# Kernel optimization log

Measured on AMD Instinct MI355X. Metric: run time of the kernel, lower is better.

The kernel has to match this reference:

```python
import jax, jax.numpy as jnp
import numpy as np

W_RNN = 768
DEC_H = 256
TAGS = 2
TAG_EM = 32


def setup_inputs() -> dict:
    key = jax.random.key(0)
    ks = jax.random.split(key, 8)
    B, T = 64, 512
    in_size = W_RNN + TAG_EM  # 800
    aff_in = W_RNN + DEC_H    # 1024
    sents_vec = jax.random.normal(ks[0], (B, T, W_RNN), dtype=jnp.float32)
    mask_cls = jnp.ones((B, T), dtype=jnp.float32)
    # xavier-uniform-ish init for weights, zeros for biases (matches param_init)
    def xavier(k, shape):
        fan_in, fan_out = shape[1], shape[0]
        lim = float(np.sqrt(6.0 / (fan_in + fan_out)))
        return jax.random.uniform(k, shape, jnp.float32, -lim, lim)
    Wih = xavier(ks[1], (4 * DEC_H, in_size))
    Whh = xavier(ks[2], (4 * DEC_H, DEC_H))
    bih = jnp.zeros((4 * DEC_H,), jnp.float32)
    bhh = jnp.zeros((4 * DEC_H,), jnp.float32)
    Waff = xavier(ks[3], (TAGS, aff_in))
    baff = jnp.zeros((TAGS,), jnp.float32)
    tag_em = xavier(ks[4], (TAGS, TAG_EM))
    return {"sents_vec": sents_vec, "mask_cls": mask_cls, "Wih": Wih,
            "Whh": Whh, "bih": bih, "bhh": bhh, "Waff": Waff,
            "baff": baff, "tag_em": tag_em}


def reference(sents_vec, mask_cls, Wih, Whh, bih, bhh, Waff, baff, tag_em):
    # Dropout is treated in eval mode (identity), as is standard for a
    # deterministic correctness baseline.
    B, T, D = sents_vec.shape
    H = DEC_H
    h0 = jnp.zeros((B, H), sents_vec.dtype)
    go = jnp.zeros((B, TAG_EM), sents_vec.dtype)

    Hs = jnp.swapaxes(sents_vec, 0, 1)        # [T, B, D]
    Ms = jnp.swapaxes(mask_cls, 0, 1)[..., None]  # [T, B, 1]

    def step(carry, xs):
        h, c, yem = carry
        Hi, mi = xs
        x = jnp.concatenate([yem, Hi], axis=1)            # [B, 800]
        gates = x @ Wih.T + h @ Whh.T + (bih + bhh)       # [B, 4H]
        i_g, f_g, g_g, o_g = jnp.split(gates, 4, axis=1)  # torch LSTMCell order
        c_new = jax.nn.sigmoid(f_g) * c + jax.nn.sigmoid(i_g) * jnp.tanh(g_g)
        h_new = jax.nn.sigmoid(o_g) * jnp.tanh(c_new)
        score = jnp.concatenate([h_new, Hi], axis=1) @ Waff.T + baff  # [B, TAGS]
        pred = jnp.argmax(score, axis=-1)                 # [B]
        yem_new = tag_em[pred]                            # [B, TAG_EM]
        h_out = h_new * mi + h * (1.0 - mi)
        c_out = c_new * mi + c * (1.0 - mi)
        return (h_out, c_out, yem_new), score

    _, scores = jax.lax.scan(step, (h0, h0, go), (Hs, Ms))  # [T, B, TAGS]
    scores = jnp.swapaxes(scores, 0, 1)                      # [B, T, TAGS]
    return jax.nn.log_softmax(scores, axis=2)
```

## Files before the change

kernel.cpp:

```cpp
#include <hip/hip_runtime.h>
#include <cstdint>
#include <cstddef>

#define TT 512
#define BB 64
#define HH 256
#define NG 1024
#define DI 768
#define KY 32

#define LDP 56

typedef __attribute__((ext_vector_type(8))) short bfrag_t;
typedef __attribute__((ext_vector_type(4))) float f4_t;

__device__ __forceinline__ float sigf(float x) {
    return __fdividef(1.f, 1.f + __expf(-x));
}
__device__ __forceinline__ float tanhfast(float x) {
    return fmaf(2.f, sigf(2.f * x), -1.f);
}
__device__ __forceinline__ unsigned short bf_hi(float x) {
    return (unsigned short)(__float_as_uint(x) >> 16);
}
__device__ __forceinline__ float bf_hi_f(float x) {
    return __uint_as_float(__float_as_uint(x) & 0xffff0000u);
}

__global__ __launch_bounds__(256) void kgemm2(
    const float* __restrict__ sents, const float* __restrict__ Wih,
    const float* __restrict__ bih, const float* __restrict__ bhh,
    float* __restrict__ gpre, int t0)
{
    __shared__ unsigned short Ah[128 * LDP], Al[128 * LDP];
    __shared__ unsigned short Bh[128 * LDP], Bl[128 * LDP];

    const int tid = threadIdx.x;
    const int nb = blockIdx.x;
    const int mb = blockIdx.y;
    const int wv = tid >> 6, lane = tid & 63;
    const int wm = (wv >> 1) * 64, wn = (wv & 1) * 64;
    const int fl = lane & 15, quad = lane >> 4;

    f4_t acc[4][4];
#pragma unroll
    for (int mi = 0; mi < 4; ++mi)
#pragma unroll
        for (int ni = 0; ni < 4; ++ni) acc[mi][ni] = (f4_t)0.f;

    const int sr = tid >> 1, sk = (tid & 1) * 16;
    const int gr = mb * 128 + sr;
    const float* aptr = sents + ((size_t)(gr & 63) * TT + t0 + (gr >> 6)) * DI + sk;
    const float* bptr = Wih + (size_t)(nb * 128 + sr) * 800 + KY + sk;

    for (int k0 = 0; k0 < DI; k0 += 32) {
        float4 av[4], bv[4];
#pragma unroll
        for (int i = 0; i < 4; ++i) {
            av[i] = *(const float4*)(aptr + k0 + i * 4);
            bv[i] = *(const float4*)(bptr + k0 + i * 4);
        }
        __syncthreads();
#pragma unroll
        for (int i = 0; i < 4; ++i) {
            ushort4 h4, l4;
            h4.x = bf_hi(av[i].x); l4.x = bf_hi(av[i].x - bf_hi_f(av[i].x));
            h4.y = bf_hi(av[i].y); l4.y = bf_hi(av[i].y - bf_hi_f(av[i].y));
            h4.z = bf_hi(av[i].z); l4.z = bf_hi(av[i].z - bf_hi_f(av[i].z));
            h4.w = bf_hi(av[i].w); l4.w = bf_hi(av[i].w - bf_hi_f(av[i].w));
            *(ushort4*)&Ah[sr * LDP + sk + i * 4] = h4;
            *(ushort4*)&Al[sr * LDP + sk + i * 4] = l4;
            h4.x = bf_hi(bv[i].x); l4.x = bf_hi(bv[i].x - bf_hi_f(bv[i].x));
            h4.y = bf_hi(bv[i].y); l4.y = bf_hi(bv[i].y - bf_hi_f(bv[i].y));
            h4.z = bf_hi(bv[i].z); l4.z = bf_hi(bv[i].z - bf_hi_f(bv[i].z));
            h4.w = bf_hi(bv[i].w); l4.w = bf_hi(bv[i].w - bf_hi_f(bv[i].w));
            *(ushort4*)&Bh[sr * LDP + sk + i * 4] = h4;
            *(ushort4*)&Bl[sr * LDP + sk + i * 4] = l4;
        }
        __syncthreads();

        bfrag_t ah[4], al2[4], bh[4], bl2[4];
#pragma unroll
        for (int mi = 0; mi < 4; ++mi) {
            int row = wm + mi * 16 + fl;
            ah[mi]  = *(const bfrag_t*)&Ah[row * LDP + quad * 8];
            al2[mi] = *(const bfrag_t*)&Al[row * LDP + quad * 8];
        }
#pragma unroll
        for (int ni = 0; ni < 4; ++ni) {
            int col = wn + ni * 16 + fl;
            bh[ni]  = *(const bfrag_t*)&Bh[col * LDP + quad * 8];
            bl2[ni] = *(const bfrag_t*)&Bl[col * LDP + quad * 8];
        }
#pragma unroll
        for (int mi = 0; mi < 4; ++mi)
#pragma unroll
            for (int ni = 0; ni < 4; ++ni) {
                acc[mi][ni] = __builtin_amdgcn_mfma_f32_16x16x32_bf16(
                    ah[mi], bh[ni], acc[mi][ni], 0, 0, 0);
                acc[mi][ni] = __builtin_amdgcn_mfma_f32_16x16x32_bf16(
                    ah[mi], bl2[ni], acc[mi][ni], 0, 0, 0);
                acc[mi][ni] = __builtin_amdgcn_mfma_f32_16x16x32_bf16(
                    al2[mi], bh[ni], acc[mi][ni], 0, 0, 0);
            }
    }

#pragma unroll
    for (int ni = 0; ni < 4; ++ni) {
        int gcol = nb * 128 + wn + ni * 16 + fl;
        float bias = bih[gcol] + bhh[gcol];
#pragma unroll
        for (int mi = 0; mi < 4; ++mi) {
            int grow = mb * 128 + wm + mi * 16 + quad * 4;
#pragma unroll
            for (int r = 0; r < 4; ++r)
                gpre[(size_t)(grow + r) * NG + gcol] = acc[mi][ni][r] + bias;
        }
    }
}

__global__ __launch_bounds__(256) void kshi(
    const float* __restrict__ sents, const float* __restrict__ Waff,
    const float* __restrict__ baff, float* __restrict__ shi, int t0)
{
    const int tid = threadIdx.x;
    const int lane = tid & 63;
    const int r = blockIdx.x * 4 + (tid >> 6);
    const int b = r & 63, tl = r >> 6;
    const float* hi = sents + ((size_t)b * TT + t0 + tl) * DI;
    float p0 = 0.f, p1 = 0.f;
#pragma unroll
    for (int kk = 0; kk < 12; ++kk) {
        int k = kk * 64 + lane;
        float x = hi[k];
        p0 = fmaf(x, Waff[HH + k], p0);
        p1 = fmaf(x, Waff[NG + HH + k], p1);
    }
#pragma unroll
    for (int off = 32; off >= 1; off >>= 1) {
        p0 += __shfl_xor(p0, off, 64);
        p1 += __shfl_xor(p1, off, 64);
    }
    if (lane == 0) {
        shi[(size_t)r * 2 + 0] = p0 + baff[0];
        shi[(size_t)r * 2 + 1] = p1 + baff[1];
    }
}

__global__ void kinit(unsigned long long* __restrict__ hbox) {
    hbox[(size_t)blockIdx.x * 512 + threadIdx.x] = 0ull;
}

__global__ __launch_bounds__(512, 1) void krec3(
    const float* __restrict__ gpre,
    const float* __restrict__ shi,
    const float* __restrict__ Whh,
    const float* __restrict__ mask,
    float* __restrict__ out,
    float* __restrict__ sh, float* __restrict__ sc, int* __restrict__ sp,
    unsigned long long* __restrict__ hbox,
    const float* __restrict__ Wih, const float* __restrict__ tag,
    const float* __restrict__ Waff,
    int t0, int Tc, int first)
{
    const int blk = blockIdx.x;
    const int g = blk >> 6, b = blk & 63;
    const int tid = threadIdx.x;
    const int w = tid >> 6, lane = tid & 63;
    const int jl = lane & 7, kq = lane >> 3;
    const int jh = w * 8 + jl;
    const int jglob = g * 64 + jh;

    __shared__ float hk[8 * 36];
    __shared__ float hnS[HH];
    __shared__ float P[2][4][64];
    __shared__ float tg[2][KY];
    __shared__ float red[8][2];

    float4 wreg[4][8];
#pragma unroll
    for (int gt = 0; gt < 4; ++gt) {
        const float4* src = (const float4*)(Whh + (size_t)(gt * HH + jglob) * HH + kq * 32);
#pragma unroll
        for (int kk = 0; kk < 8; ++kk) wreg[gt][kk] = src[kk];
    }

    const int sdim = w * 32 + (lane & 31);
    const int stag = lane >> 5;
    const float waffR = Waff[(size_t)stag * NG + sdim];

    if (tid < 2 * KY) tg[tid >> 5][tid & 31] = tag[tid];
    __syncthreads();
    {
        int r = tid >> 8, rem = tid & 255, gt = rem >> 6, j2 = rem & 63;
        int row = gt * HH + g * 64 + j2;
        const float4* wr = (const float4*)(Wih + (size_t)row * 800);
        float s = 0.f;
#pragma unroll
        for (int kk = 0; kk < 8; ++kk) {
            float4 v = wr[kk];
            s = fmaf(v.x, tg[r][kk * 4 + 0], s);
            s = fmaf(v.y, tg[r][kk * 4 + 1], s);
            s = fmaf(v.z, tg[r][kk * 4 + 2], s);
            s = fmaf(v.w, tg[r][kk * 4 + 3], s);
        }
        P[r][gt][j2] = s;
    }

    float creg; int pred;
    if (first) {
        creg = 0.f; pred = -1;
        if (tid < 72) ((float4*)hk)[tid] = make_float4(0.f, 0.f, 0.f, 0.f);
    } else {
        creg = sc[(size_t)b * HH + jglob];
        pred = sp[b];
        if (tid < HH) hk[(tid >> 5) * 36 + (tid & 31)] = sh[(size_t)b * HH + tid];
    }
    __syncthreads();

    float cgp0, cgp1, cgp2, cgp3, cmi, cs0, cs1;
    {
        const float* gp = gpre + ((size_t)0 * BB + b) * NG;
        cgp0 = gp[0 * HH + jglob]; cgp1 = gp[1 * HH + jglob];
        cgp2 = gp[2 * HH + jglob]; cgp3 = gp[3 * HH + jglob];
        cmi = mask[(size_t)b * TT + t0];
        const float* s2 = shi + ((size_t)0 * BB + b) * 2;
        cs0 = s2[0]; cs1 = s2[1];
    }

    for (int tl = 0; tl < Tc; ++tl) {
        const int t = t0 + tl;
        const int p = t & 1;

        float pv0 = 0.f, pv1 = 0.f, pv2 = 0.f, pv3 = 0.f;
        if (pred >= 0) {
            pv0 = P[pred][0][jh]; pv1 = P[pred][1][jh];
            pv2 = P[pred][2][jh]; pv3 = P[pred][3][jh];
        }

        float a0 = 0.f, a1 = 0.f, a2 = 0.f, a3 = 0.f;
        const float4* h4 = (const float4*)(hk + kq * 36);
#pragma unroll
        for (int kk = 0; kk < 8; ++kk) {
            float4 hv = h4[kk];
            a0 = fmaf(wreg[0][kk].x, hv.x, a0); a0 = fmaf(wreg[0][kk].y, hv.y, a0);
            a0 = fmaf(wreg[0][kk].z, hv.z, a0); a0 = fmaf(wreg[0][kk].w, hv.w, a0);
            a1 = fmaf(wreg[1][kk].x, hv.x, a1); a1 = fmaf(wreg[1][kk].y, hv.y, a1);
            a1 = fmaf(wreg[1][kk].z, hv.z, a1); a1 = fmaf(wreg[1][kk].w, hv.w, a1);
            a2 = fmaf(wreg[2][kk].x, hv.x, a2); a2 = fmaf(wreg[2][kk].y, hv.y, a2);
            a2 = fmaf(wreg[2][kk].z, hv.z, a2); a2 = fmaf(wreg[2][kk].w, hv.w, a2);
            a3 = fmaf(wreg[3][kk].x, hv.x, a3); a3 = fmaf(wreg[3][kk].y, hv.y, a3);
            a3 = fmaf(wreg[3][kk].z, hv.z, a3); a3 = fmaf(wreg[3][kk].w, hv.w, a3);
        }
        a0 += __shfl_xor(a0, 8, 64); a0 += __shfl_xor(a0, 16, 64); a0 += __shfl_xor(a0, 32, 64);
        a1 += __shfl_xor(a1, 8, 64); a1 += __shfl_xor(a1, 16, 64); a1 += __shfl_xor(a1, 32, 64);
        a2 += __shfl_xor(a2, 8, 64); a2 += __shfl_xor(a2, 16, 64); a2 += __shfl_xor(a2, 32, 64);
        a3 += __shfl_xor(a3, 8, 64); a3 += __shfl_xor(a3, 16, 64); a3 += __shfl_xor(a3, 32, 64);

        float gi = a0 + cgp0 + pv0;
        float gf = a1 + cgp1 + pv1;
        float gg = a2 + cgp2 + pv2;
        float go = a3 + cgp3 + pv3;
        float ig = sigf(gi), fg = sigf(gf);
        float g2 = tanhfast(gg), og = sigf(go);
        float cn = fmaf(fg, creg, ig * g2);
        float hn = og * tanhfast(cn);
        float mi = cmi;
        float s2v0 = cs0, s2v1 = cs1;
        creg = cn * mi + creg * (1.f - mi);

        if (kq == 0) {
            unsigned long long wd =
                ((unsigned long long)__float_as_uint(hn) << 32) | (unsigned)(t + 1);
            __hip_atomic_store(&hbox[((size_t)(p * BB + b) * 4 + g) * 64 + jh], wd,
                               __ATOMIC_RELAXED, __HIP_MEMORY_SCOPE_AGENT);
            hnS[jglob] = hn;
        }

        if (tl + 1 < Tc) {
            const float* gp2 = gpre + ((size_t)(tl + 1) * BB + b) * NG;
            cgp0 = gp2[0 * HH + jglob]; cgp1 = gp2[1 * HH + jglob];
            cgp2 = gp2[2 * HH + jglob]; cgp3 = gp2[3 * HH + jglob];
            cmi = mask[(size_t)b * TT + t + 1];
            const float* s2n = shi + ((size_t)(tl + 1) * BB + b) * 2;
            cs0 = s2n[0]; cs1 = s2n[1];
        }

        if (tid < 192) {
            int pg = (g + 1 + (tid >> 6)) & 3, j2 = tid & 63;
            const unsigned long long* wp = &hbox[((size_t)(p * BB + b) * 4 + pg) * 64 + j2];
            unsigned long long wv;
            do {
                wv = __hip_atomic_load(wp, __ATOMIC_RELAXED, __HIP_MEMORY_SCOPE_AGENT);
            } while ((unsigned)wv != (unsigned)(t + 1));
            hnS[pg * 64 + j2] = __uint_as_float((unsigned)(wv >> 32));
        }
        __syncthreads();

        if (tid < HH) {
            int idx = (tid >> 5) * 36 + (tid & 31);
            float hold = hk[idx];
            hk[idx] = hnS[tid] * mi + hold * (1.f - mi);
        }
        float prod = hnS[sdim] * waffR;
        prod += __shfl_xor(prod, 1, 64);
        prod += __shfl_xor(prod, 2, 64);
        prod += __shfl_xor(prod, 4, 64);
        prod += __shfl_xor(prod, 8, 64);
        prod += __shfl_xor(prod, 16, 64);
        if ((lane & 31) == 0) red[w][stag] = prod;
        __syncthreads();

        float s0 = red[0][0];
        s0 += red[1][0]; s0 += red[2][0]; s0 += red[3][0];
        s0 += red[4][0]; s0 += red[5][0]; s0 += red[6][0]; s0 += red[7][0];
        float s1 = red[0][1];
        s1 += red[1][1]; s1 += red[2][1]; s1 += red[3][1];
        s1 += red[4][1]; s1 += red[5][1]; s1 += red[6][1]; s1 += red[7][1];
        float ts0 = s0 + s2v0, ts1 = s1 + s2v1;
        pred = (ts1 > ts0) ? 1 : 0;
        if (g == 0 && tid == 0) {
            float m = fmaxf(ts0, ts1);
            float lse = m + log1pf(expf(-fabsf(ts0 - ts1)));
            float* op = out + ((size_t)b * TT + t) * 2;
            op[0] = ts0 - lse; op[1] = ts1 - lse;
        }
    }

    if (kq == 0) {
        sh[(size_t)b * HH + jglob] = hk[(jglob >> 5) * 36 + (jglob & 31)];
        sc[(size_t)b * HH + jglob] = creg;
    }
    if (g == 0 && tid == 0) sp[b] = pred;
}

extern "C" void kernel_launch(void* const* d_in, const int* in_sizes, int n_in,
                              void* d_out, int out_size, void* d_ws, size_t ws_size,
                              hipStream_t stream) {
    (void)in_sizes; (void)n_in; (void)out_size;
    const float* sents = (const float*)d_in[0];
    const float* mask  = (const float*)d_in[1];
    const float* Wih   = (const float*)d_in[2];
    const float* Whh   = (const float*)d_in[3];
    const float* bih   = (const float*)d_in[4];
    const float* bhh   = (const float*)d_in[5];
    const float* Waff  = (const float*)d_in[6];
    const float* baff  = (const float*)d_in[7];
    const float* tag   = (const float*)d_in[8];
    float* out = (float*)d_out;

    const size_t fixed = (size_t)BB * HH * 4 * 2
                       + BB * 4
                       + (size_t)2 * BB * 4 * 64 * 8
                       + 4096;
    int Tc = 8;
    const int cands[7] = {512, 256, 128, 64, 32, 16, 8};
    for (int i = 0; i < 7; ++i) {
        size_t need = (size_t)cands[i] * BB * NG * 4
                    + (size_t)cands[i] * BB * 2 * 4
                    + fixed;
        if (need <= ws_size) { Tc = cands[i]; break; }
    }

    char* wsp = (char*)d_ws;
    float* gpre = (float*)wsp; wsp += (size_t)Tc * BB * NG * 4;
    float* shiw = (float*)wsp; wsp += (size_t)Tc * BB * 2 * 4;
    float* shst = (float*)wsp; wsp += (size_t)BB * HH * 4;
    float* scst = (float*)wsp; wsp += (size_t)BB * HH * 4;
    int*   spst = (int*)wsp;   wsp += BB * 4;
    unsigned long long* hbox = (unsigned long long*)wsp;

    kinit<<<dim3(64), 512, 0, stream>>>(hbox);

    const int nch = TT / Tc;
    for (int c = 0; c < nch; ++c) {
        const int t0 = c * Tc;
        kgemm2<<<dim3(8, Tc * 64 / 128), 256, 0, stream>>>(sents, Wih, bih, bhh, gpre, t0);
        kshi<<<dim3(Tc * 16), 256, 0, stream>>>(sents, Waff, baff, shiw, t0);
        krec3<<<dim3(256), 512, 0, stream>>>(gpre, shiw, Whh, mask, out,
                                             shst, scst, spst, hbox,
                                             Wih, tag, Waff, t0, Tc, (c == 0) ? 1 : 0);
    }
}
```

Before: 1.289 ms.

## Fuse next-chunk input GEMM and score projection into the recurrence launch

Replaces the per-chunk sequence of three kernels (input-gate GEMM, tag-score projection, recurrence) with one kernel launch per chunk. Blocks 0-255 run the recurrence for the current chunk while the extra blocks compute the GEMM and score projection for the next chunk into double-buffered workspace. The aim is to hide the input-projection work behind the latency-bound serial recurrence. In exchange, chunk size is capped at 32 steps, which means more launches and repeated per-chunk setup (Whh register reload, P table). The merged kernel may also raise register pressure. The cross-block spin-wait relies on the 256 recurrence blocks all being resident at the same time, which depends on them being dispatched first.

```diff
diff --git a/kernel.cpp b/kernel.cpp
--- a/kernel.cpp
+++ b/kernel.cpp
@@ -151,187 +151,303 @@
     hbox[(size_t)blockIdx.x * 512 + threadIdx.x] = 0ull;
 }
 
-__global__ __launch_bounds__(512, 1) void krec3(
-    const float* __restrict__ gpre,
-    const float* __restrict__ shi,
-    const float* __restrict__ Whh,
-    const float* __restrict__ mask,
+__global__ __launch_bounds__(512, 1) void kstep(
+    const float* __restrict__ sents,
+    const float* __restrict__ Wih, const float* __restrict__ bih,
+    const float* __restrict__ bhh, const float* __restrict__ Whh,
+    const float* __restrict__ mask, const float* __restrict__ Waff,
+    const float* __restrict__ baff, const float* __restrict__ tag,
     float* __restrict__ out,
+    const float* __restrict__ gpreR, float* __restrict__ gpreW,
+    const float* __restrict__ shiR, float* __restrict__ shiW,
     float* __restrict__ sh, float* __restrict__ sc, int* __restrict__ sp,
     unsigned long long* __restrict__ hbox,
-    const float* __restrict__ Wih, const float* __restrict__ tag,
-    const float* __restrict__ Waff,
-    int t0, int Tc, int first)
+    int t0, int Tc, int first, int doNext)
 {
-    const int blk = blockIdx.x;
-    const int g = blk >> 6, b = blk & 63;
+    __shared__ union {
+        struct { unsigned short Ah[128 * LDP], Al[128 * LDP],
+                                Bh[128 * LDP], Bl[128 * LDP]; } g;
+        struct { float hk[8 * 36]; float hnS[HH]; float P[2][4][64];
+                 float tg[2][KY]; float red[8][2]; } r;
+    } sm;
+
     const int tid = threadIdx.x;
-    const int w = tid >> 6, lane = tid & 63;
-    const int jl = lane & 7, kq = lane >> 3;
-    const int jh = w * 8 + jl;
-    const int jglob = g * 64 + jh;
-
-    __shared__ float hk[8 * 36];
-    __shared__ float hnS[HH];
-    __shared__ float P[2][4][64];
-    __shared__ float tg[2][KY];
-    __shared__ float red[8][2];
-
-    float4 wreg[4][8];
-#pragma unroll
-    for (int gt = 0; gt < 4; ++gt) {
-        const float4* src = (const float4*)(Whh + (size_t)(gt * HH + jglob) * HH + kq * 32);
-#pragma unroll
-        for (int kk = 0; kk < 8; ++kk) wreg[gt][kk] = src[kk];
-    }
-
-    const int sdim = w * 32 + (lane & 31);
-    const int stag = lane >> 5;
-    const float waffR = Waff[(size_t)stag * NG + sdim];
-
-    if (tid < 2 * KY) tg[tid >> 5][tid & 31] = tag[tid];
-    __syncthreads();
-    {
-        int r = tid >> 8, rem = tid & 255, gt = rem >> 6, j2 = rem & 63;
-        int row = gt * HH + g * 64 + j2;
-        const float4* wr = (const float4*)(Wih + (size_t)row * 800);
-        float s = 0.f;
-#pragma unroll
-        for (int kk = 0; kk < 8; ++kk) {
-            float4 v = wr[kk];
-            s = fmaf(v.x, tg[r][kk * 4 + 0], s);
-            s = fmaf(v.y, tg[r][kk * 4 + 1], s);
-            s = fmaf(v.z, tg[r][kk * 4 + 2], s);
-            s = fmaf(v.w, tg[r][kk * 4 + 3], s);
-        }
-        P[r][gt][j2] = s;
-    }
-
-    float creg; int pred;
-    if (first) {
-        creg = 0.f; pred = -1;
-        if (tid < 72) ((float4*)hk)[tid] = make_float4(0.f, 0.f, 0.f, 0.f);
+    const int gemmBase = 256;
+    const int shiBase  = 256 + Tc * 4;
+
+    if (blockIdx.x < 256) {
+        const int blk = blockIdx.x;
+        const int g = blk >> 6, b = blk & 63;
+        const int w = tid >> 6, lane = tid & 63;
+        const int jl = lane & 7, kq = lane >> 3;
+        const int jh = w * 8 + jl;
+        const int jglob = g * 64 + jh;
+
+        float4 wreg[4][8];
+#pragma unroll
+        for (int gt = 0; gt < 4; ++gt) {
+            const float4* src = (const float4*)(Whh + (size_t)(gt * HH + jglob) * HH + kq * 32);
+#pragma unroll
+            for (int kk = 0; kk < 8; ++kk) wreg[gt][kk] = src[kk];
+        }
+
+        const int sdim = w * 32 + (lane & 31);
+        const int stag = lane >> 5;
+        const float waffR = Waff[(size_t)stag * NG + sdim];
+
+        if (tid < 2 * KY) sm.r.tg[tid >> 5][tid & 31] = tag[tid];
+        __syncthreads();
+        {
+            int r = tid >> 8, rem = tid & 255, gt = rem >> 6, j2 = rem & 63;
+            int row = gt * HH + g * 64 + j2;
+            const float4* wr = (const float4*)(Wih + (size_t)row * 800);
+            float s = 0.f;
+#pragma unroll
+            for (int kk = 0; kk < 8; ++kk) {
+                float4 v = wr[kk];
+                s = fmaf(v.x, sm.r.tg[r][kk * 4 + 0], s);
+                s = fmaf(v.y, sm.r.tg[r][kk * 4 + 1], s);
+                s = fmaf(v.z, sm.r.tg[r][kk * 4 + 2], s);
+                s = fmaf(v.w, sm.r.tg[r][kk * 4 + 3], s);
+            }
+            sm.r.P[r][gt][j2] = s;
+        }
+
+        float creg; int pred;
+        if (first) {
+            creg = 0.f; pred = -1;
+            if (tid < 72) ((float4*)sm.r.hk)[tid] = make_float4(0.f, 0.f, 0.f, 0.f);
+        } else {
+            creg = sc[(size_t)b * HH + jglob];
+            pred = sp[b];
+            if (tid < HH) sm.r.hk[(tid >> 5) * 36 + (tid & 31)] = sh[(size_t)b * HH + tid];
+        }
+        __syncthreads();
+
+        float cgp0, cgp1, cgp2, cgp3, cmi, cs0, cs1;
+        {
+            const float* gp = gpreR + (size_t)b * NG;
+            cgp0 = gp[0 * HH + jglob]; cgp1 = gp[1 * HH + jglob];
+            cgp2 = gp[2 * HH + jglob]; cgp3 = gp[3 * HH + jglob];
+            cmi = mask[(size_t)b * TT + t0];
+            const float* s2 = shiR + (size_t)b * 2;
+            cs0 = s2[0]; cs1 = s2[1];
+        }
+
+        for (int tl = 0; tl < Tc; ++tl) {
+            const int t = t0 + tl;
+            const int p = t & 1;
+
+            float pv0 = 0.f, pv1 = 0.f, pv2 = 0.f, pv3 = 0.f;
+            if (pred >= 0) {
+                pv0 = sm.r.P[pred][0][jh]; pv1 = sm.r.P[pred][1][jh];
+                pv2 = sm.r.P[pred][2][jh]; pv3 = sm.r.P[pred][3][jh];
+            }
+
+            float a0 = 0.f, a1 = 0.f, a2 = 0.f, a3 = 0.f;
+            const float4* h4 = (const float4*)(sm.r.hk + kq * 36);
+#pragma unroll
+            for (int kk = 0; kk < 8; ++kk) {
+                float4 hv = h4[kk];
+                a0 = fmaf(wreg[0][kk].x, hv.x, a0); a0 = fmaf(wreg[0][kk].y, hv.y, a0);
+                a0 = fmaf(wreg[0][kk].z, hv.z, a0); a0 = fmaf(wreg[0][kk].w, hv.w, a0);
+                a1 = fmaf(wreg[1][kk].x, hv.x, a1); a1 = fmaf(wreg[1][kk].y, hv.y, a1);
+                a1 = fmaf(wreg[1][kk].z, hv.z, a1); a1 = fmaf(wreg[1][kk].w, hv.w, a1);
+                a2 = fmaf(wreg[2][kk].x, hv.x, a2); a2 = fmaf(wreg[2][kk].y, hv.y, a2);
+                a2 = fmaf(wreg[2][kk].z, hv.z, a2); a2 = fmaf(wreg[2][kk].w, hv.w, a2);
+                a3 = fmaf(wreg[3][kk].x, hv.x, a3); a3 = fmaf(wreg[3][kk].y, hv.y, a3);
+                a3 = fmaf(wreg[3][kk].z, hv.z, a3); a3 = fmaf(wreg[3][kk].w, hv.w, a3);
+            }
+            a0 += __shfl_xor(a0, 8, 64); a0 += __shfl_xor(a0, 16, 64); a0 += __shfl_xor(a0, 32, 64);
+            a1 += __shfl_xor(a1, 8, 64); a1 += __shfl_xor(a1, 16, 64); a1 += __shfl_xor(a1, 32, 64);
+            a2 += __shfl_xor(a2, 8, 64); a2 += __shfl_xor(a2, 16, 64); a2 += __shfl_xor(a2, 32, 64);
+            a3 += __shfl_xor(a3, 8, 64); a3 += __shfl_xor(a3, 16, 64); a3 += __shfl_xor(a3, 32, 64);
+
+            float gi = a0 + cgp0 + pv0;
+            float gf = a1 + cgp1 + pv1;
+            float gg = a2 + cgp2 + pv2;
+            float go = a3 + cgp3 + pv3;
+            float ig = sigf(gi), fg = sigf(gf);
+            float g2 = tanhfast(gg), og = sigf(go);
+            float cn = fmaf(fg, creg, ig * g2);
+            float hn = og * tanhfast(cn);
+            float mi = cmi;
+            float s2v0 = cs0, s2v1 = cs1;
+            creg = cn * mi + creg * (1.f - mi);
+
+            if (kq == 0) {
+                unsigned long long wd =
+                    ((unsigned long long)__float_as_uint(hn) << 32) | (unsigned)(t + 1);
+                __hip_atomic_store(&hbox[((size_t)(p * BB + b) * 4 + g) * 64 + jh], wd,
+                                   __ATOMIC_RELAXED, __HIP_MEMORY_SCOPE_AGENT);
+                sm.r.hnS[jglob] = hn;
+            }
+
+            if (tl + 1 < Tc) {
+                const float* gp2 = gpreR + ((size_t)(tl + 1) * BB + b) * NG;
+                cgp0 = gp2[0 * HH + jglob]; cgp1 = gp2[1 * HH + jglob];
+                cgp2 = gp2[2 * HH + jglob]; cgp3 = gp2[3 * HH + jglob];
+                cmi = mask[(size_t)b * TT + t + 1];
+                const float* s2n = shiR + ((size_t)(tl + 1) * BB + b) * 2;
+                cs0 = s2n[0]; cs1 = s2n[1];
+            }
+
+            if (tid < 192) {
+                int pg = (g + 1 + (tid >> 6)) & 3, j2 = tid & 63;
+                const unsigned long long* wp = &hbox[((size_t)(p * BB + b) * 4 + pg) * 64 + j2];
+                unsigned long long wv;
+                do {
+                    wv = __hip_atomic_load(wp, __ATOMIC_RELAXED, __HIP_MEMORY_SCOPE_AGENT);
+                } while ((unsigned)wv != (unsigned)(t + 1));
+                sm.r.hnS[pg * 64 + j2] = __uint_as_float((unsigned)(wv >> 32));
+            }
+            __syncthreads();
+
+            if (tid < HH) {
+                int idx = (tid >> 5) * 36 + (tid & 31);
+                float hold = sm.r.hk[idx];
+                sm.r.hk[idx] = sm.r.hnS[tid] * mi + hold * (1.f - mi);
+            }
+            float prod = sm.r.hnS[sdim] * waffR;
+            prod += __shfl_xor(prod, 1, 64);
+            prod += __shfl_xor(prod, 2, 64);
+            prod += __shfl_xor(prod, 4, 64);
+            prod += __shfl_xor(prod, 8, 64);
+            prod += __shfl_xor(prod, 16, 64);
+            if ((lane & 31) == 0) sm.r.red[w][stag] = prod;
+            __syncthreads();
+
+            float s0 = sm.r.red[0][0];
+            s0 += sm.r.red[1][0]; s0 += sm.r.red[2][0]; s0 += sm.r.red[3][0];
+            s0 += sm.r.red[4][0]; s0 += sm.r.red[5][0]; s0 += sm.r.red[6][0]; s0 += sm.r.red[7][0];
+            float s1 = sm.r.red[0][1];
+            s1 += sm.r.red[1][1]; s1 += sm.r.red[2][1]; s1 += sm.r.red[3][1];
+            s1 += sm.r.red[4][1]; s1 += sm.r.red[5][1]; s1 += sm.r.red[6][1]; s1 += sm.r.red[7][1];
+            float ts0 = s0 + s2v0, ts1 = s1 + s2v1;
+            pred = (ts1 > ts0) ? 1 : 0;
+            if (g == 0 && tid == 0) {
+                float m = fmaxf(ts0, ts1);
+                float lse = m + log1pf(expf(-fabsf(ts0 - ts1)));
+                float* op = out + ((size_t)b * TT + t) * 2;
+                op[0] = ts0 - lse; op[1] = ts1 - lse;
+            }
+        }
+
+        if (kq == 0) {
+            sh[(size_t)b * HH + jglob] = sm.r.hk[(jglob >> 5) * 36 + (jglob & 31)];
+            sc[(size_t)b * HH + jglob] = creg;
+        }
+        if (g == 0 && tid == 0) sp[b] = pred;
+
+    } else if (blockIdx.x < shiBase) {
+        if (!doNext) return;
+        const int gb = blockIdx.x - gemmBase;
+        const int nb = gb & 7, mb = gb >> 3;
+        const int t0n = t0 + Tc;
+        const int wv = tid >> 6, lane = tid & 63;
+        const int wm = (wv >> 2) * 64, wn = (wv & 3) * 32;
+        const int fl = lane & 15, quad = lane >> 4;
+
+        f4_t acc[4][2];
+#pragma unroll
+        for (int mi = 0; mi < 4; ++mi)
+#pragma unroll
+            for (int ni = 0; ni < 2; ++ni) acc[mi][ni] = (f4_t)0.f;
+
+        const int sr = tid >> 2, sk = (tid & 3) * 8;
+        const int gr = mb * 128 + sr;
+        const float* aptr = sents + ((size_t)(gr & 63) * TT + t0n + (gr >> 6)) * DI + sk;
+        const float* bptr = Wih + (size_t)(nb * 128 + sr) * 800 + KY + sk;
+
+        for (int k0 = 0; k0 < DI; k0 += 32) {
+            float4 av[2], bv[2];
+            av[0] = *(const float4*)(aptr + k0);
+            av[1] = *(const float4*)(aptr + k0 + 4);
+            bv[0] = *(const float4*)(bptr + k0);
+            bv[1] = *(const float4*)(bptr + k0 + 4);
+            __syncthreads();
+#pragma unroll
+            for (int i = 0; i < 2; ++i) {
+                ushort4 h4, l4;
+                h4.x = bf_hi(av[i].x); l4.x = bf_hi(av[i].x - bf_hi_f(av[i].x));
+                h4.y = bf_hi(av[i].y); l4.y = bf_hi(av[i].y - bf_hi_f(av[i].y));
+                h4.z = bf_hi(av[i].z); l4.z = bf_hi(av[i].z - bf_hi_f(av[i].z));
+                h4.w = bf_hi(av[i].w); l4.w = bf_hi(av[i].w - bf_hi_f(av[i].w));
+                *(ushort4*)&sm.g.Ah[sr * LDP + sk + i * 4] = h4;
+                *(ushort4*)&sm.g.Al[sr * LDP + sk + i * 4] = l4;
+                h4.x = bf_hi(bv[i].x); l4.x = bf_hi(bv[i].x - bf_hi_f(bv[i].x));
+                h4.y = bf_hi(bv[i].y); l4.y = bf_hi(bv[i].y - bf_hi_f(bv[i].y));
+                h4.z = bf_hi(bv[i].z); l4.z = bf_hi(bv[i].z - bf_hi_f(bv[i].z));
+                h4.w = bf_hi(bv[i].w); l4.w = bf_hi(bv[i].w - bf_hi_f(bv[i].w));
+                *(ushort4*)&sm.g.Bh[sr * LDP + sk + i * 4] = h4;
+                *(ushort4*)&sm.g.Bl[sr * LDP + sk + i * 4] = l4;
+            }
+            __syncthreads();
+
+            bfrag_t ah[4], al2[4], bh[2], bl2[2];
+#pragma unroll
+            for (int mi = 0; mi < 4; ++mi) {
+                int row = wm + mi * 16 + fl;
+                ah[mi]  = *(const bfrag_t*)&sm.g.Ah[row * LDP + quad * 8];
+                al2[mi] = *(const bfrag_t*)&sm.g.Al[row * LDP + quad * 8];
+            }
+#pragma unroll
+            for (int ni = 0; ni < 2; ++ni) {
+                int col = wn + ni * 16 + fl;
+                bh[ni]  = *(const bfrag_t*)&sm.g.Bh[col * LDP + quad * 8];
+                bl2[ni] = *(const bfrag_t*)&sm.g.Bl[col * LDP + quad * 8];
+            }
+#pragma unroll
+            for (int mi = 0; mi < 4; ++mi)
+#pragma unroll
+                for (int ni = 0; ni < 2; ++ni) {
+                    acc[mi][ni] = __builtin_amdgcn_mfma_f32_16x16x32_bf16(
+                        ah[mi], bh[ni], acc[mi][ni], 0, 0, 0);
+                    acc[mi][ni] = __builtin_amdgcn_mfma_f32_16x16x32_bf16(
+                        ah[mi], bl2[ni], acc[mi][ni], 0, 0, 0);
+                    acc[mi][ni] = __builtin_amdgcn_mfma_f32_16x16x32_bf16(
+                        al2[mi], bh[ni], acc[mi][ni], 0, 0, 0);
+                }
+        }
+
+#pragma unroll
+        for (int ni = 0; ni < 2; ++ni) {
+            int gcol = nb * 128 + wn + ni * 16 + fl;
+            float bias = bih[gcol] + bhh[gcol];
+#pragma unroll
+            for (int mi = 0; mi < 4; ++mi) {
+                int grow = mb * 128 + wm + mi * 16 + quad * 4;
+#pragma unroll
+                for (int r = 0; r < 4; ++r)
+                    gpreW[(size_t)(grow + r) * NG + gcol] = acc[mi][ni][r] + bias;
+            }
+        }
+
     } else {
-        creg = sc[(size_t)b * HH + jglob];
-        pred = sp[b];
-        if (tid < HH) hk[(tid >> 5) * 36 + (tid & 31)] = sh[(size_t)b * HH + tid];
-    }
-    __syncthreads();
-
-    float cgp0, cgp1, cgp2, cgp3, cmi, cs0, cs1;
-    {
-        const float* gp = gpre + ((size_t)0 * BB + b) * NG;
-        cgp0 = gp[0 * HH + jglob]; cgp1 = gp[1 * HH + jglob];
-        cgp2 = gp[2 * HH + jglob]; cgp3 = gp[3 * HH + jglob];
-        cmi = mask[(size_t)b * TT + t0];
-        const float* s2 = shi + ((size_t)0 * BB + b) * 2;
-        cs0 = s2[0]; cs1 = s2[1];
-    }
-
-    for (int tl = 0; tl < Tc; ++tl) {
-        const int t = t0 + tl;
-        const int p = t & 1;
-
-        float pv0 = 0.f, pv1 = 0.f, pv2 = 0.f, pv3 = 0.f;
-        if (pred >= 0) {
-            pv0 = P[pred][0][jh]; pv1 = P[pred][1][jh];
-            pv2 = P[pred][2][jh]; pv3 = P[pred][3][jh];
-        }
-
-        float a0 = 0.f, a1 = 0.f, a2 = 0.f, a3 = 0.f;
-        const float4* h4 = (const float4*)(hk + kq * 36);
-#pragma unroll
-        for (int kk = 0; kk < 8; ++kk) {
-            float4 hv = h4[kk];
-            a0 = fmaf(wreg[0][kk].x, hv.x, a0); a0 = fmaf(wreg[0][kk].y, hv.y, a0);
-            a0 = fmaf(wreg[0][kk].z, hv.z, a0); a0 = fmaf(wreg[0][kk].w, hv.w, a0);
-            a1 = fmaf(wreg[1][kk].x, hv.x, a1); a1 = fmaf(wreg[1][kk].y, hv.y, a1);
-            a1 = fmaf(wreg[1][kk].z, hv.z, a1); a1 = fmaf(wreg[1][kk].w, hv.w, a1);
-            a2 = fmaf(wreg[2][kk].x, hv.x, a2); a2 = fmaf(wreg[2][kk].y, hv.y, a2);
-            a2 = fmaf(wreg[2][kk].z, hv.z, a2); a2 = fmaf(wreg[2][kk].w, hv.w, a2);
-            a3 = fmaf(wreg[3][kk].x, hv.x, a3); a3 = fmaf(wreg[3][kk].y, hv.y, a3);
-            a3 = fmaf(wreg[3][kk].z, hv.z, a3); a3 = fmaf(wreg[3][kk].w, hv.w, a3);
-        }
-        a0 += __shfl_xor(a0, 8, 64); a0 += __shfl_xor(a0, 16, 64); a0 += __shfl_xor(a0, 32, 64);
-        a1 += __shfl_xor(a1, 8, 64); a1 += __shfl_xor(a1, 16, 64); a1 += __shfl_xor(a1, 32, 64);
-        a2 += __shfl_xor(a2, 8, 64); a2 += __shfl_xor(a2, 16, 64); a2 += __shfl_xor(a2, 32, 64);
-        a3 += __shfl_xor(a3, 8, 64); a3 += __shfl_xor(a3, 16, 64); a3 += __shfl_xor(a3, 32, 64);
-
-        float gi = a0 + cgp0 + pv0;
-        float gf = a1 + cgp1 + pv1;
-        float gg = a2 + cgp2 + pv2;
-        float go = a3 + cgp3 + pv3;
-        float ig = sigf(gi), fg = sigf(gf);
-        float g2 = tanhfast(gg), og = sigf(go);
-        float cn = fmaf(fg, creg, ig * g2);
-        float hn = og * tanhfast(cn);
-        float mi = cmi;
-        float s2v0 = cs0, s2v1 = cs1;
-        creg = cn * mi + creg * (1.f - mi);
-
-        if (kq == 0) {
-            unsigned long long wd =
-                ((unsigned long long)__float_as_uint(hn) << 32) | (unsigned)(t + 1);
-            __hip_atomic_store(&hbox[((size_t)(p * BB + b) * 4 + g) * 64 + jh], wd,
-                               __ATOMIC_RELAXED, __HIP_MEMORY_SCOPE_AGENT);
-            hnS[jglob] = hn;
-        }
-
-        if (tl + 1 < Tc) {
-            const float* gp2 = gpre + ((size_t)(tl + 1) * BB + b) * NG;
-            cgp0 = gp2[0 * HH + jglob]; cgp1 = gp2[1 * HH + jglob];
-            cgp2 = gp2[2 * HH + jglob]; cgp3 = gp2[3 * HH + jglob];
-            cmi = mask[(size_t)b * TT + t + 1];
-            const float* s2n = shi + ((size_t)(tl + 1) * BB + b) * 2;
-            cs0 = s2n[0]; cs1 = s2n[1];
-        }
-
-        if (tid < 192) {
-            int pg = (g + 1 + (tid >> 6)) & 3, j2 = tid & 63;
-            const unsigned long long* wp = &hbox[((size_t)(p * BB + b) * 4 + pg) * 64 + j2];
-            unsigned long long wv;
-            do {
-                wv = __hip_atomic_load(wp, __ATOMIC_RELAXED, __HIP_MEMORY_SCOPE_AGENT);
-            } while ((unsigned)wv != (unsigned)(t + 1));
-            hnS[pg * 64 + j2] = __uint_as_float((unsigned)(wv >> 32));
-        }
-        __syncthreads();
-
-        if (tid < HH) {
-            int idx = (tid >> 5) * 36 + (tid & 31);
-            float hold = hk[idx];
-            hk[idx] = hnS[tid] * mi + hold * (1.f - mi);
-        }
-        float prod = hnS[sdim] * waffR;
-        prod += __shfl_xor(prod, 1, 64);
-        prod += __shfl_xor(prod, 2, 64);
-        prod += __shfl_xor(prod, 4, 64);
-        prod += __shfl_xor(prod, 8, 64);
-        prod += __shfl_xor(prod, 16, 64);
-        if ((lane & 31) == 0) red[w][stag] = prod;
-        __syncthreads();
-
-        float s0 = red[0][0];
-        s0 += red[1][0]; s0 += red[2][0]; s0 += red[3][0];
-        s0 += red[4][0]; s0 += red[5][0]; s0 += red[6][0]; s0 += red[7][0];
-        float s1 = red[0][1];
-        s1 += red[1][1]; s1 += red[2][1]; s1 += red[3][1];
-        s1 += red[4][1]; s1 += red[5][1]; s1 += red[6][1]; s1 += red[7][1];
-        float ts0 = s0 + s2v0, ts1 = s1 + s2v1;
-        pred = (ts1 > ts0) ? 1 : 0;
-        if (g == 0 && tid == 0) {
-            float m = fmaxf(ts0, ts1);
-            float lse = m + log1pf(expf(-fabsf(ts0 - ts1)));
-            float* op = out + ((size_t)b * TT + t) * 2;
-            op[0] = ts0 - lse; op[1] = ts1 - lse;
-        }
-    }
-
-    if (kq == 0) {
-        sh[(size_t)b * HH + jglob] = hk[(jglob >> 5) * 36 + (jglob & 31)];
-        sc[(size_t)b * HH + jglob] = creg;
-    }
-    if (g == 0 && tid == 0) sp[b] = pred;
+        if (!doNext) return;
+        const int wv = tid >> 6, lane = tid & 63;
+        const int r = (blockIdx.x - shiBase) * 8 + wv;
+        const int b = r & 63, tl = r >> 6;
+        const int t0n = t0 + Tc;
+        const float* hi = sents + ((size_t)b * TT + t0n + tl) * DI;
+        float p0 = 0.f, p1 = 0.f;
+#pragma unroll
+        for (int kk = 0; kk < 12; ++kk) {
+            int k = kk * 64 + lane;
+            float x = hi[k];
+            p0 = fmaf(x, Waff[HH + k], p0);
+            p1 = fmaf(x, Waff[NG + HH + k], p1);
+        }
+#pragma unroll
+        for (int off = 32; off >= 1; off >>= 1) {
+            p0 += __shfl_xor(p0, off, 64);
+            p1 += __shfl_xor(p1, off, 64);
+        }
+        if (lane == 0) {
+            shiW[(size_t)r * 2 + 0] = p0 + baff[0];
+            shiW[(size_t)r * 2 + 1] = p1 + baff[1];
+        }
+    }
 }
 
 extern "C" void kernel_launch(void* const* d_in, const int* in_sizes, int n_in,
@@ -354,31 +470,38 @@
                        + (size_t)2 * BB * 4 * 64 * 8
                        + 4096;
     int Tc = 8;
-    const int cands[7] = {512, 256, 128, 64, 32, 16, 8};
-    for (int i = 0; i < 7; ++i) {
-        size_t need = (size_t)cands[i] * BB * NG * 4
-                    + (size_t)cands[i] * BB * 2 * 4
+    const int cands[4] = {32, 16, 8, 4};
+    for (int i = 0; i < 4; ++i) {
+        size_t need = 2 * ((size_t)cands[i] * BB * NG * 4 + (size_t)cands[i] * BB * 2 * 4)
                     + fixed;
         if (need <= ws_size) { Tc = cands[i]; break; }
     }
 
     char* wsp = (char*)d_ws;
-    float* gpre = (float*)wsp; wsp += (size_t)Tc * BB * NG * 4;
-    float* shiw = (float*)wsp; wsp += (size_t)Tc * BB * 2 * 4;
+    float* gpre0 = (float*)wsp; wsp += (size_t)Tc * BB * NG * 4;
+    float* gpre1 = (float*)wsp; wsp += (size_t)Tc * BB * NG * 4;
+    float* shi0 = (float*)wsp; wsp += (size_t)Tc * BB * 2 * 4;
+    float* shi1 = (float*)wsp; wsp += (size_t)Tc * BB * 2 * 4;
     float* shst = (float*)wsp; wsp += (size_t)BB * HH * 4;
     float* scst = (float*)wsp; wsp += (size_t)BB * HH * 4;
     int*   spst = (int*)wsp;   wsp += BB * 4;
     unsigned long long* hbox = (unsigned long long*)wsp;
 
+    float* gbuf[2] = {gpre0, gpre1};
+    float* sbuf[2] = {shi0, shi1};
+
     kinit<<<dim3(64), 512, 0, stream>>>(hbox);
+    kgemm2<<<dim3(8, Tc * 64 / 128), 256, 0, stream>>>(sents, Wih, bih, bhh, gpre0, 0);
+    kshi<<<dim3(Tc * 16), 256, 0, stream>>>(sents, Waff, baff, shi0, 0);
 
     const int nch = TT / Tc;
+    const int grid = 256 + Tc * 4 + Tc * 8;
     for (int c = 0; c < nch; ++c) {
         const int t0 = c * Tc;
-        kgemm2<<<dim3(8, Tc * 64 / 128), 256, 0, stream>>>(sents, Wih, bih, bhh, gpre, t0);
-        kshi<<<dim3(Tc * 16), 256, 0, stream>>>(sents, Waff, baff, shiw, t0);
-        krec3<<<dim3(256), 512, 0, stream>>>(gpre, shiw, Whh, mask, out,
-                                             shst, scst, spst, hbox,
-                                             Wih, tag, Waff, t0, Tc, (c == 0) ? 1 : 0);
-    }
-}
+        kstep<<<dim3(grid), 512, 0, stream>>>(
+            sents, Wih, bih, bhh, Whh, mask, Waff, baff, tag, out,
+            gbuf[c & 1], gbuf[(c + 1) & 1], sbuf[c & 1], sbuf[(c + 1) & 1],
+            shst, scst, spst, hbox,
+            t0, Tc, (c == 0) ? 1 : 0, (c + 1 < nch) ? 1 : 0);
+    }
+}
```

After: 2.200 ms. 70.7% more time.
